# Optimization experiments

Hardware: AMD Instinct MI355X
Metric: run time of the kernel (lower is better)

The kernel has to match this reference:

```python
import jax, jax.numpy as jnp
import numpy as np

H = 32   # rnn_hidden_dim * num_directions
L = 2    # num_layers
F = 1    # num_features
B, T = 2048, 1024


def _xavier(key, shape):
    lim = np.sqrt(6.0 / (shape[0] + shape[1])).astype(np.float32)
    return jax.random.uniform(key, shape, jnp.float32, -lim, lim)


def _lstm_uniform(key, shape):
    lim = np.float32(1.0 / np.sqrt(H))
    return jax.random.uniform(key, shape, jnp.float32, -lim, lim)


def setup_inputs() -> dict:
    key = jax.random.key(0)
    ks = jax.random.split(key, 12)
    return {
        "padded_sequence": jax.random.normal(ks[0], (B, T, F), jnp.float32),
        "z": jax.random.normal(ks[1], (B, H), jnp.float32),
        "lengths": jnp.full((B,), T, jnp.int32),
        # LSTM layer 0 (input size F)
        "w_ih0": _lstm_uniform(ks[2], (4 * H, F)),
        "w_hh0": _lstm_uniform(ks[3], (4 * H, H)),
        "b_ih0": _lstm_uniform(ks[4], (4 * H,)).reshape(4 * H),
        "b_hh0": _lstm_uniform(ks[5], (4 * H,)).reshape(4 * H),
        # LSTM layer 1 (input size H)
        "w_ih1": _lstm_uniform(ks[6], (4 * H, H)),
        "w_hh1": _lstm_uniform(ks[7], (4 * H, H)),
        "b_ih1": _lstm_uniform(ks[8], (4 * H,)).reshape(4 * H),
        "b_hh1": _lstm_uniform(ks[9], (4 * H,)).reshape(4 * H),
        # output projection (xavier weight, bias filled 0.01 per _init_weights)
        "w_out": _xavier(ks[10], (F, H)),
        "b_out": jnp.full((F,), 0.01, jnp.float32),
    }


def _cell(x, h, c, w_ih, w_hh, b):
    # PyTorch LSTM gate order: i, f, g, o
    gates = x @ w_ih.T + h @ w_hh.T + b  # (B, 4H)
    i, f, g, o = jnp.split(gates, 4, axis=-1)
    c_new = jax.nn.sigmoid(f) * c + jax.nn.sigmoid(i) * jnp.tanh(g)
    h_new = jax.nn.sigmoid(o) * jnp.tanh(c_new)
    return h_new, c_new


def reference(padded_sequence, z, lengths, w_ih0, w_hh0, b_ih0, b_hh0,
              w_ih1, w_hh1, b_ih1, b_hh1, w_out, b_out):
    b_sz, n_steps, f = padded_sequence.shape
    b0 = b_ih0 + b_hh0
    b1 = b_ih1 + b_hh1
    pred0 = jnp.zeros((b_sz, f), padded_sequence.dtype)
    # hidden = (z.repeat(L,1,1), z.repeat(L,1,1)): both layers' h and c start as z
    init = (pred0, z, z, z, z)

    def step(carry, _):
        pred, h0, c0, h1, c1 = carry
        h0n, c0n = _cell(pred, h0, c0, w_ih0, w_hh0, b0)
        h1n, c1n = _cell(h0n, h1, c1, w_ih1, w_hh1, b1)
        pred_n = h1n @ w_out.T + b_out  # (B, F)
        return (pred_n, h0n, c0n, h1n, c1n), pred_n

    _, preds = jax.lax.scan(step, init, None, length=n_steps)  # (T, B, F)
    recovered = jnp.transpose(preds, (1, 0, 2))  # (B, T, F)
    loss = jnp.mean((padded_sequence - recovered) ** 2)
    return loss, recovered
```

## Files before the change

kernel.cpp:

```cpp
#include <hip/hip_runtime.h>

#define NB 2048
#define NT 1024

typedef _Float16 half2_t __attribute__((ext_vector_type(2)));
union F4H { float4 f; half2_t h[4]; };

__device__ __forceinline__ float sig_fast(float x) {
    return __builtin_amdgcn_rcpf(1.0f + __builtin_amdgcn_exp2f(-1.4426950408889634f * x));
}
__device__ __forceinline__ float tanh_fast(float x) {
    return fmaf(2.0f, __builtin_amdgcn_rcpf(1.0f + __builtin_amdgcn_exp2f(-2.8853900817779268f * x)), -1.0f);
}

__global__ void zero_loss_kernel(float* out) { out[0] = 0.0f; }

#define LD4(P, i) (*(const float4*)&(P)[i])
#define FDOT(acc, w, hh) acc = __builtin_amdgcn_fdot2((w), (hh), (acc), false)
#define PINH(v) asm volatile("" : "+v"(v))

#define CVTQ(n0, n1, p, i) { float4 r_ = LD4(p, i); \
  n0.x=(_Float16)r_.x; n0.y=(_Float16)r_.y; n1.x=(_Float16)r_.z; n1.y=(_Float16)r_.w; }

#define DECL_ROWH(n, src, row) \
  half2_t n##0,n##1,n##2,n##3,n##4,n##5,n##6,n##7,n##8,n##9,n##10,n##11,n##12,n##13,n##14,n##15; \
  CVTQ(n##0, n##1, src,(row)*32+ 0) CVTQ(n##2, n##3, src,(row)*32+ 4) \
  CVTQ(n##4, n##5, src,(row)*32+ 8) CVTQ(n##6, n##7, src,(row)*32+12) \
  CVTQ(n##8, n##9, src,(row)*32+16) CVTQ(n##10,n##11,src,(row)*32+20) \
  CVTQ(n##12,n##13,src,(row)*32+24) CVTQ(n##14,n##15,src,(row)*32+28) \
  PINH(n##0); PINH(n##1); PINH(n##2); PINH(n##3); PINH(n##4); PINH(n##5); PINH(n##6); PINH(n##7); \
  PINH(n##8); PINH(n##9); PINH(n##10); PINH(n##11); PINH(n##12); PINH(n##13); PINH(n##14); PINH(n##15);

#define DOT16(a0, a1, n, U0, U1, U2, U3) \
  FDOT(a0, n##0,  (U0).h[0]); FDOT(a1, n##1,  (U0).h[1]); \
  FDOT(a0, n##2,  (U0).h[2]); FDOT(a1, n##3,  (U0).h[3]); \
  FDOT(a0, n##4,  (U1).h[0]); FDOT(a1, n##5,  (U1).h[1]); \
  FDOT(a0, n##6,  (U1).h[2]); FDOT(a1, n##7,  (U1).h[3]); \
  FDOT(a0, n##8,  (U2).h[0]); FDOT(a1, n##9,  (U2).h[1]); \
  FDOT(a0, n##10, (U2).h[2]); FDOT(a1, n##11, (U2).h[3]); \
  FDOT(a0, n##12, (U3).h[0]); FDOT(a1, n##13, (U3).h[1]); \
  FDOT(a0, n##14, (U3).h[2]); FDOT(a1, n##15, (U3).h[3]);

__global__ __launch_bounds__(128) __attribute__((amdgpu_waves_per_eu(4, 4)))
void decoder_lstm_kernel(const float* __restrict__ seq,
                         const float* __restrict__ z,
                         const float* __restrict__ w_ih0,
                         const float* __restrict__ w_hh0,
                         const float* __restrict__ b_ih0,
                         const float* __restrict__ b_hh0,
                         const float* __restrict__ w_ih1,
                         const float* __restrict__ w_hh1,
                         const float* __restrict__ b_ih1,
                         const float* __restrict__ b_hh1,
                         const float* __restrict__ w_out,
                         const float* __restrict__ b_out,
                         float* __restrict__ out)
{
    const int tid = threadIdx.x;
    const int w   = tid >> 6;
    const int l   = tid & 63;
    const int q   = l >> 4;
    const int u   = 16 * w + (l & 15);
    const int R   = q * 32 + u;
    const int b   = blockIdx.x;

    __shared__ __align__(16) _Float16 h0buf[2][32];
    __shared__ __align__(16) _Float16 h1buf[2][32];
    __shared__ float pb[2];

    DECL_ROWH(w0, w_hh0, R)
    DECL_ROWH(wi, w_ih1, R)
    DECL_ROWH(wh, w_hh1, R)

    const float wih0R = w_ih0[R];
    const float bias0 = b_ih0[R] + b_hh0[R];
    const float bias1 = b_ih1[R] + b_hh1[R];

    const float m2 = (q == 2) ? 1.0f : 0.0f;
    const float eM = (q == 2) ? -2.8853900817779268f : -1.4426950408889634f;

    const float wOutL = (l < 16) ? w_out[u] : 0.0f;
    const float bOut  = b_out[0];

    const float cz = z[(size_t)b * 32 + u];
    float c0 = cz, c1 = cz;
    if (l < 16) { h0buf[0][u] = (_Float16)cz; h1buf[0][u] = (_Float16)cz; }
    float pred = 0.0f, sse = 0.0f, xreg = 0.0f;

    const float* seq_b = seq + (size_t)b * NT;
    float* out_b = out + 1 + (size_t)b * NT;

    __syncthreads();

    for (int t = 0; t < NT; ++t) {
        const int par = t & 1;
        if (w == 0 && (t & 63) == 0) xreg = seq_b[t + l];

        F4H U0, U1, U2, U3;
        {
            const float4* p0 = (const float4*)h0buf[par];
            U0.f = p0[0]; U1.f = p0[1]; U2.f = p0[2]; U3.f = p0[3];
        }

        float a0 = fmaf(pred, wih0R, bias0), a1 = 0.0f;
        DOT16(a0, a1, w0, U0, U1, U2, U3);
        float v  = a0 + a1;
        float s  = __builtin_amdgcn_rcpf(1.0f + __builtin_amdgcn_exp2f(eM * v));
        float av = fmaf(m2, s - 1.0f, s);

        float x16 = __shfl_xor(av, 16);
        float x32 = __shfl_xor(av, 32);
        float x48 = __shfl_xor(av, 48);
        c0 = fmaf(x16, c0, av * x32);
        float h0n = x48 * tanh_fast(c0);
        if (l < 16) h0buf[par ^ 1][u] = (_Float16)h0n;
        __syncthreads();

        F4H V0, V1, V2, V3, X0, X1, X2, X3;
        {
            const float4* p  = (const float4*)h0buf[par ^ 1];
            const float4* p1 = (const float4*)h1buf[par];
            V0.f = p[0];  V1.f = p[1];  V2.f = p[2];  V3.f = p[3];
            X0.f = p1[0]; X1.f = p1[1]; X2.f = p1[2]; X3.f = p1[3];
        }
        float d0 = bias1, d1 = 0.0f, d2 = 0.0f, d3 = 0.0f;
        DOT16(d0, d1, wi, V0, V1, V2, V3);
        DOT16(d2, d3, wh, X0, X1, X2, X3);
        float v1  = (d0 + d1) + (d2 + d3);
        float s1  = __builtin_amdgcn_rcpf(1.0f + __builtin_amdgcn_exp2f(eM * v1));
        float av1 = fmaf(m2, s1 - 1.0f, s1);

        float y16 = __shfl_xor(av1, 16);
        float y32 = __shfl_xor(av1, 32);
        float y48 = __shfl_xor(av1, 48);
        c1 = fmaf(y16, c1, av1 * y32);
        float h1n = y48 * tanh_fast(c1);
        if (l < 16) h1buf[par ^ 1][u] = (_Float16)h1n;

        float term = wOutL * h1n;
        term += __shfl_xor(term, 1);
        term += __shfl_xor(term, 2);
        term += __shfl_xor(term, 4);
        term += __shfl_xor(term, 8);
        if (l == 0) pb[w] = term;
        __syncthreads();

        pred = bOut + pb[0] + pb[1];

        if (w == 0) {
            out_b[t] = pred;
            float d    = xreg - pred;
            float dsel = ((t & 63) == l) ? d : 0.0f;
            sse = fmaf(dsel, d, sse);
        }
    }

    if (w == 0) {
        sse += __shfl_xor(sse, 1);
        sse += __shfl_xor(sse, 2);
        sse += __shfl_xor(sse, 4);
        sse += __shfl_xor(sse, 8);
        sse += __shfl_xor(sse, 16);
        sse += __shfl_xor(sse, 32);
        if (l == 0) atomicAdd(out, sse * (1.0f / ((float)NB * (float)NT)));
    }
}

extern "C" void kernel_launch(void* const* d_in, const int* in_sizes, int n_in,
                              void* d_out, int out_size, void* d_ws, size_t ws_size,
                              hipStream_t stream) {
    const float* seq   = (const float*)d_in[0];
    const float* z     = (const float*)d_in[1];
    const float* w_ih0 = (const float*)d_in[3];
    const float* w_hh0 = (const float*)d_in[4];
    const float* b_ih0 = (const float*)d_in[5];
    const float* b_hh0 = (const float*)d_in[6];
    const float* w_ih1 = (const float*)d_in[7];
    const float* w_hh1 = (const float*)d_in[8];
    const float* b_ih1 = (const float*)d_in[9];
    const float* b_hh1 = (const float*)d_in[10];
    const float* w_out = (const float*)d_in[11];
    const float* b_out = (const float*)d_in[12];
    float* out = (float*)d_out;

    hipLaunchKernelGGL(zero_loss_kernel, dim3(1), dim3(1), 0, stream, out);
    hipLaunchKernelGGL(decoder_lstm_kernel, dim3(NB), dim3(128), 0, stream,
                       seq, z, w_ih0, w_hh0, b_ih0, b_hh0,
                       w_ih1, w_hh1, b_ih1, b_hh1, w_out, b_out, out);
}
```

Measured before the change: 1.140 ms.

## Stream fp16 recurrent weights from global each step instead of pinning in registers

Adds a prep kernel that converts the three recurrent weight matrices to fp16 and packs them per gate row into a workspace blob. The main kernel then reloads each row's 96 halves from global/L1 every timestep instead of holding 48 packed registers for the whole loop. The aim is to cut VGPR pressure, at the price of extra per-step memory loads on the serial critical path. The asm barrier on the pointer keeps the compiler from hoisting the loads out of the loop.

```diff
diff --git a/kernel.cpp b/kernel.cpp
--- a/kernel.cpp
+++ b/kernel.cpp
@@ -6,54 +6,41 @@
 typedef _Float16 half2_t __attribute__((ext_vector_type(2)));
 union F4H { float4 f; half2_t h[4]; };
 
-__device__ __forceinline__ float sig_fast(float x) {
-    return __builtin_amdgcn_rcpf(1.0f + __builtin_amdgcn_exp2f(-1.4426950408889634f * x));
-}
 __device__ __forceinline__ float tanh_fast(float x) {
     return fmaf(2.0f, __builtin_amdgcn_rcpf(1.0f + __builtin_amdgcn_exp2f(-2.8853900817779268f * x)), -1.0f);
 }
 
 __global__ void zero_loss_kernel(float* out) { out[0] = 0.0f; }
 
-#define LD4(P, i) (*(const float4*)&(P)[i])
+__global__ void prep_weights(const float* __restrict__ w_hh0,
+                             const float* __restrict__ w_ih1,
+                             const float* __restrict__ w_hh1,
+                             _Float16* __restrict__ blob) {
+    int i = blockIdx.x * blockDim.x + threadIdx.x;
+    if (i < 128 * 32) {
+        int R = i >> 5, k = i & 31;
+        blob[R * 96 +      k] = (_Float16)w_hh0[i];
+        blob[R * 96 + 32 + k] = (_Float16)w_ih1[i];
+        blob[R * 96 + 64 + k] = (_Float16)w_hh1[i];
+    }
+}
+
 #define FDOT(acc, w, hh) acc = __builtin_amdgcn_fdot2((w), (hh), (acc), false)
-#define PINH(v) asm volatile("" : "+v"(v))
-
-#define CVTQ(n0, n1, p, i) { float4 r_ = LD4(p, i); \
-  n0.x=(_Float16)r_.x; n0.y=(_Float16)r_.y; n1.x=(_Float16)r_.z; n1.y=(_Float16)r_.w; }
-
-#define DECL_ROWH(n, src, row) \
-  half2_t n##0,n##1,n##2,n##3,n##4,n##5,n##6,n##7,n##8,n##9,n##10,n##11,n##12,n##13,n##14,n##15; \
-  CVTQ(n##0, n##1, src,(row)*32+ 0) CVTQ(n##2, n##3, src,(row)*32+ 4) \
-  CVTQ(n##4, n##5, src,(row)*32+ 8) CVTQ(n##6, n##7, src,(row)*32+12) \
-  CVTQ(n##8, n##9, src,(row)*32+16) CVTQ(n##10,n##11,src,(row)*32+20) \
-  CVTQ(n##12,n##13,src,(row)*32+24) CVTQ(n##14,n##15,src,(row)*32+28) \
-  PINH(n##0); PINH(n##1); PINH(n##2); PINH(n##3); PINH(n##4); PINH(n##5); PINH(n##6); PINH(n##7); \
-  PINH(n##8); PINH(n##9); PINH(n##10); PINH(n##11); PINH(n##12); PINH(n##13); PINH(n##14); PINH(n##15);
-
-#define DOT16(a0, a1, n, U0, U1, U2, U3) \
-  FDOT(a0, n##0,  (U0).h[0]); FDOT(a1, n##1,  (U0).h[1]); \
-  FDOT(a0, n##2,  (U0).h[2]); FDOT(a1, n##3,  (U0).h[3]); \
-  FDOT(a0, n##4,  (U1).h[0]); FDOT(a1, n##5,  (U1).h[1]); \
-  FDOT(a0, n##6,  (U1).h[2]); FDOT(a1, n##7,  (U1).h[3]); \
-  FDOT(a0, n##8,  (U2).h[0]); FDOT(a1, n##9,  (U2).h[1]); \
-  FDOT(a0, n##10, (U2).h[2]); FDOT(a1, n##11, (U2).h[3]); \
-  FDOT(a0, n##12, (U3).h[0]); FDOT(a1, n##13, (U3).h[1]); \
-  FDOT(a0, n##14, (U3).h[2]); FDOT(a1, n##15, (U3).h[3]);
+#define DOT4W(a0, a1, W, U) \
+  FDOT(a0, (W).h[0], (U).h[0]); FDOT(a1, (W).h[1], (U).h[1]); \
+  FDOT(a0, (W).h[2], (U).h[2]); FDOT(a1, (W).h[3], (U).h[3]);
 
 __global__ __launch_bounds__(128) __attribute__((amdgpu_waves_per_eu(4, 4)))
 void decoder_lstm_kernel(const float* __restrict__ seq,
                          const float* __restrict__ z,
                          const float* __restrict__ w_ih0,
-                         const float* __restrict__ w_hh0,
                          const float* __restrict__ b_ih0,
                          const float* __restrict__ b_hh0,
-                         const float* __restrict__ w_ih1,
-                         const float* __restrict__ w_hh1,
                          const float* __restrict__ b_ih1,
                          const float* __restrict__ b_hh1,
                          const float* __restrict__ w_out,
                          const float* __restrict__ b_out,
+                         const _Float16* __restrict__ blob,
                          float* __restrict__ out)
 {
     const int tid = threadIdx.x;
@@ -68,9 +55,7 @@
     __shared__ __align__(16) _Float16 h1buf[2][32];
     __shared__ float pb[2];
 
-    DECL_ROWH(w0, w_hh0, R)
-    DECL_ROWH(wi, w_ih1, R)
-    DECL_ROWH(wh, w_hh1, R)
+    const _Float16* wp = blob + R * 96;
 
     const float wih0R = w_ih0[R];
     const float bias0 = b_ih0[R] + b_hh0[R];
@@ -94,19 +79,34 @@
 
     for (int t = 0; t < NT; ++t) {
         const int par = t & 1;
+
+        const _Float16* wq = wp;
+        asm("" : "+v"(wq));
+
         if (w == 0 && (t & 63) == 0) xreg = seq_b[t + l];
 
+        F4H Wa, Wb, Wc, Wd;
+        Wa.f = *(const float4*)(wq +  0);
+        Wb.f = *(const float4*)(wq +  8);
+        Wc.f = *(const float4*)(wq + 16);
+        Wd.f = *(const float4*)(wq + 24);
+
         F4H U0, U1, U2, U3;
-        {
-            const float4* p0 = (const float4*)h0buf[par];
-            U0.f = p0[0]; U1.f = p0[1]; U2.f = p0[2]; U3.f = p0[3];
-        }
+        { const float4* p0 = (const float4*)h0buf[par];
+          U0.f = p0[0]; U1.f = p0[1]; U2.f = p0[2]; U3.f = p0[3]; }
 
         float a0 = fmaf(pred, wih0R, bias0), a1 = 0.0f;
-        DOT16(a0, a1, w0, U0, U1, U2, U3);
+        DOT4W(a0, a1, Wa, U0); DOT4W(a0, a1, Wb, U1);
+        DOT4W(a0, a1, Wc, U2); DOT4W(a0, a1, Wd, U3);
         float v  = a0 + a1;
         float s  = __builtin_amdgcn_rcpf(1.0f + __builtin_amdgcn_exp2f(eM * v));
         float av = fmaf(m2, s - 1.0f, s);
+
+        F4H Ia, Ib, Ic, Id;
+        Ia.f = *(const float4*)(wq + 32);
+        Ib.f = *(const float4*)(wq + 40);
+        Ic.f = *(const float4*)(wq + 48);
+        Id.f = *(const float4*)(wq + 56);
 
         float x16 = __shfl_xor(av, 16);
         float x32 = __shfl_xor(av, 32);
@@ -116,16 +116,24 @@
         if (l < 16) h0buf[par ^ 1][u] = (_Float16)h0n;
         __syncthreads();
 
+        F4H Ha, Hb, Hc, Hd;
+        Ha.f = *(const float4*)(wq + 64);
+        Hb.f = *(const float4*)(wq + 72);
+        Hc.f = *(const float4*)(wq + 80);
+        Hd.f = *(const float4*)(wq + 88);
+
         F4H V0, V1, V2, V3, X0, X1, X2, X3;
-        {
-            const float4* p  = (const float4*)h0buf[par ^ 1];
-            const float4* p1 = (const float4*)h1buf[par];
-            V0.f = p[0];  V1.f = p[1];  V2.f = p[2];  V3.f = p[3];
-            X0.f = p1[0]; X1.f = p1[1]; X2.f = p1[2]; X3.f = p1[3];
-        }
-        float d0 = bias1, d1 = 0.0f, d2 = 0.0f, d3 = 0.0f;
-        DOT16(d0, d1, wi, V0, V1, V2, V3);
-        DOT16(d2, d3, wh, X0, X1, X2, X3);
+        { const float4* p  = (const float4*)h0buf[par ^ 1];
+          const float4* p1 = (const float4*)h1buf[par];
+          V0.f = p[0];  V1.f = p[1];  V2.f = p[2];  V3.f = p[3];
+          X0.f = p1[0]; X1.f = p1[1]; X2.f = p1[2]; X3.f = p1[3]; }
+
+        float d0 = bias1, d1 = 0.0f;
+        DOT4W(d0, d1, Ia, V0); DOT4W(d0, d1, Ib, V1);
+        DOT4W(d0, d1, Ic, V2); DOT4W(d0, d1, Id, V3);
+        float d2 = 0.0f, d3 = 0.0f;
+        DOT4W(d2, d3, Ha, X0); DOT4W(d2, d3, Hb, X1);
+        DOT4W(d2, d3, Hc, X2); DOT4W(d2, d3, Hd, X3);
         float v1  = (d0 + d1) + (d2 + d3);
         float s1  = __builtin_amdgcn_rcpf(1.0f + __builtin_amdgcn_exp2f(eM * v1));
         float av1 = fmaf(m2, s1 - 1.0f, s1);
@@ -182,9 +190,12 @@
     const float* w_out = (const float*)d_in[11];
     const float* b_out = (const float*)d_in[12];
     float* out = (float*)d_out;
+    _Float16* blob = (_Float16*)d_ws;
 
     hipLaunchKernelGGL(zero_loss_kernel, dim3(1), dim3(1), 0, stream, out);
+    hipLaunchKernelGGL(prep_weights, dim3(16), dim3(256), 0, stream,
+                       w_hh0, w_ih1, w_hh1, blob);
     hipLaunchKernelGGL(decoder_lstm_kernel, dim3(NB), dim3(128), 0, stream,
-                       seq, z, w_ih0, w_hh0, b_ih0, b_hh0,
-                       w_ih1, w_hh1, b_ih1, b_hh1, w_out, b_out, out);
-}
+                       seq, z, w_ih0, b_ih0, b_hh0, b_ih1, b_hh1,
+                       w_out, b_out, blob, out);
+}
```

Result: slower. 2.733 ms (+139.7%).

## Split each gate row's K dimension across two lanes with 256-thread blocks

Applied to the files above, without the earlier changes.

Each block now uses four waves instead of two. Each gate row's 32-element dot product is split into two 16-element halves held by paired lanes, and the halves are combined with an extra cross-lane shuffle before the activations. This halves the per-thread weight registers and dot-product chain length, shortening the serial per-timestep latency. The cost is twice the threads per batch element, an extra shuffle per layer, and more waves taking part in each block barrier.

```diff
diff --git a/kernel.cpp b/kernel.cpp
--- a/kernel.cpp
+++ b/kernel.cpp
@@ -6,9 +6,6 @@
 typedef _Float16 half2_t __attribute__((ext_vector_type(2)));
 union F4H { float4 f; half2_t h[4]; };
 
-__device__ __forceinline__ float sig_fast(float x) {
-    return __builtin_amdgcn_rcpf(1.0f + __builtin_amdgcn_exp2f(-1.4426950408889634f * x));
-}
 __device__ __forceinline__ float tanh_fast(float x) {
     return fmaf(2.0f, __builtin_amdgcn_rcpf(1.0f + __builtin_amdgcn_exp2f(-2.8853900817779268f * x)), -1.0f);
 }
@@ -17,31 +14,22 @@
 
 #define LD4(P, i) (*(const float4*)&(P)[i])
 #define FDOT(acc, w, hh) acc = __builtin_amdgcn_fdot2((w), (hh), (acc), false)
-#define PINH(v) asm volatile("" : "+v"(v))
 
 #define CVTQ(n0, n1, p, i) { float4 r_ = LD4(p, i); \
   n0.x=(_Float16)r_.x; n0.y=(_Float16)r_.y; n1.x=(_Float16)r_.z; n1.y=(_Float16)r_.w; }
 
-#define DECL_ROWH(n, src, row) \
-  half2_t n##0,n##1,n##2,n##3,n##4,n##5,n##6,n##7,n##8,n##9,n##10,n##11,n##12,n##13,n##14,n##15; \
-  CVTQ(n##0, n##1, src,(row)*32+ 0) CVTQ(n##2, n##3, src,(row)*32+ 4) \
-  CVTQ(n##4, n##5, src,(row)*32+ 8) CVTQ(n##6, n##7, src,(row)*32+12) \
-  CVTQ(n##8, n##9, src,(row)*32+16) CVTQ(n##10,n##11,src,(row)*32+20) \
-  CVTQ(n##12,n##13,src,(row)*32+24) CVTQ(n##14,n##15,src,(row)*32+28) \
-  PINH(n##0); PINH(n##1); PINH(n##2); PINH(n##3); PINH(n##4); PINH(n##5); PINH(n##6); PINH(n##7); \
-  PINH(n##8); PINH(n##9); PINH(n##10); PINH(n##11); PINH(n##12); PINH(n##13); PINH(n##14); PINH(n##15);
+#define DECL_HALFROW(n, src, row, kb) \
+  half2_t n##0,n##1,n##2,n##3,n##4,n##5,n##6,n##7; \
+  CVTQ(n##0, n##1, src, (row)*32 + (kb) + 0)  CVTQ(n##2, n##3, src, (row)*32 + (kb) + 4) \
+  CVTQ(n##4, n##5, src, (row)*32 + (kb) + 8)  CVTQ(n##6, n##7, src, (row)*32 + (kb) + 12)
 
-#define DOT16(a0, a1, n, U0, U1, U2, U3) \
-  FDOT(a0, n##0,  (U0).h[0]); FDOT(a1, n##1,  (U0).h[1]); \
-  FDOT(a0, n##2,  (U0).h[2]); FDOT(a1, n##3,  (U0).h[3]); \
-  FDOT(a0, n##4,  (U1).h[0]); FDOT(a1, n##5,  (U1).h[1]); \
-  FDOT(a0, n##6,  (U1).h[2]); FDOT(a1, n##7,  (U1).h[3]); \
-  FDOT(a0, n##8,  (U2).h[0]); FDOT(a1, n##9,  (U2).h[1]); \
-  FDOT(a0, n##10, (U2).h[2]); FDOT(a1, n##11, (U2).h[3]); \
-  FDOT(a0, n##12, (U3).h[0]); FDOT(a1, n##13, (U3).h[1]); \
-  FDOT(a0, n##14, (U3).h[2]); FDOT(a1, n##15, (U3).h[3]);
+#define DOT8(a0, a1, n, U0, U1) \
+  FDOT(a0, n##0, (U0).h[0]); FDOT(a1, n##1, (U0).h[1]); \
+  FDOT(a0, n##2, (U0).h[2]); FDOT(a1, n##3, (U0).h[3]); \
+  FDOT(a0, n##4, (U1).h[0]); FDOT(a1, n##5, (U1).h[1]); \
+  FDOT(a0, n##6, (U1).h[2]); FDOT(a1, n##7, (U1).h[3]);
 
-__global__ __launch_bounds__(128) __attribute__((amdgpu_waves_per_eu(4, 4)))
+__global__ __launch_bounds__(256)
 void decoder_lstm_kernel(const float* __restrict__ seq,
                          const float* __restrict__ z,
                          const float* __restrict__ w_ih0,
@@ -60,31 +48,34 @@
     const int w   = tid >> 6;
     const int l   = tid & 63;
     const int q   = l >> 4;
-    const int u   = 16 * w + (l & 15);
+    const int h   = (l >> 3) & 1;
+    const int e   = l & 7;
+    const int u   = 8 * w + e;
     const int R   = q * 32 + u;
+    const int kb  = 16 * h;
     const int b   = blockIdx.x;
 
     __shared__ __align__(16) _Float16 h0buf[2][32];
     __shared__ __align__(16) _Float16 h1buf[2][32];
-    __shared__ float pb[2];
+    __shared__ float pb[4];
 
-    DECL_ROWH(w0, w_hh0, R)
-    DECL_ROWH(wi, w_ih1, R)
-    DECL_ROWH(wh, w_hh1, R)
+    DECL_HALFROW(w0, w_hh0, R, kb)
+    DECL_HALFROW(wi, w_ih1, R, kb)
+    DECL_HALFROW(wh, w_hh1, R, kb)
 
-    const float wih0R = w_ih0[R];
-    const float bias0 = b_ih0[R] + b_hh0[R];
-    const float bias1 = b_ih1[R] + b_hh1[R];
+    const float bias0L = h ? 0.0f : (b_ih0[R] + b_hh0[R]);
+    const float bias1L = h ? 0.0f : (b_ih1[R] + b_hh1[R]);
+    const float wih0L  = h ? 0.0f : w_ih0[R];
 
     const float m2 = (q == 2) ? 1.0f : 0.0f;
     const float eM = (q == 2) ? -2.8853900817779268f : -1.4426950408889634f;
 
-    const float wOutL = (l < 16) ? w_out[u] : 0.0f;
+    const float wOutL = (l < 8) ? w_out[u] : 0.0f;
     const float bOut  = b_out[0];
 
     const float cz = z[(size_t)b * 32 + u];
     float c0 = cz, c1 = cz;
-    if (l < 16) { h0buf[0][u] = (_Float16)cz; h1buf[0][u] = (_Float16)cz; }
+    if (l < 8) { h0buf[0][u] = (_Float16)cz; h1buf[0][u] = (_Float16)cz; }
     float pred = 0.0f, sse = 0.0f, xreg = 0.0f;
 
     const float* seq_b = seq + (size_t)b * NT;
@@ -96,15 +87,14 @@
         const int par = t & 1;
         if (w == 0 && (t & 63) == 0) xreg = seq_b[t + l];
 
-        F4H U0, U1, U2, U3;
-        {
-            const float4* p0 = (const float4*)h0buf[par];
-            U0.f = p0[0]; U1.f = p0[1]; U2.f = p0[2]; U3.f = p0[3];
-        }
+        F4H U0, U1;
+        U0.f = *(const float4*)&h0buf[par][kb];
+        U1.f = *(const float4*)&h0buf[par][kb + 8];
 
-        float a0 = fmaf(pred, wih0R, bias0), a1 = 0.0f;
-        DOT16(a0, a1, w0, U0, U1, U2, U3);
-        float v  = a0 + a1;
+        float a0 = fmaf(pred, wih0L, bias0L), a1 = 0.0f;
+        DOT8(a0, a1, w0, U0, U1);
+        float v = a0 + a1;
+        v += __shfl_xor(v, 8);
         float s  = __builtin_amdgcn_rcpf(1.0f + __builtin_amdgcn_exp2f(eM * v));
         float av = fmaf(m2, s - 1.0f, s);
 
@@ -113,20 +103,20 @@
         float x48 = __shfl_xor(av, 48);
         c0 = fmaf(x16, c0, av * x32);
         float h0n = x48 * tanh_fast(c0);
-        if (l < 16) h0buf[par ^ 1][u] = (_Float16)h0n;
+        if (l < 8) h0buf[par ^ 1][u] = (_Float16)h0n;
         __syncthreads();
 
-        F4H V0, V1, V2, V3, X0, X1, X2, X3;
-        {
-            const float4* p  = (const float4*)h0buf[par ^ 1];
-            const float4* p1 = (const float4*)h1buf[par];
-            V0.f = p[0];  V1.f = p[1];  V2.f = p[2];  V3.f = p[3];
-            X0.f = p1[0]; X1.f = p1[1]; X2.f = p1[2]; X3.f = p1[3];
-        }
-        float d0 = bias1, d1 = 0.0f, d2 = 0.0f, d3 = 0.0f;
-        DOT16(d0, d1, wi, V0, V1, V2, V3);
-        DOT16(d2, d3, wh, X0, X1, X2, X3);
-        float v1  = (d0 + d1) + (d2 + d3);
+        F4H V0, V1, X0, X1;
+        V0.f = *(const float4*)&h0buf[par ^ 1][kb];
+        V1.f = *(const float4*)&h0buf[par ^ 1][kb + 8];
+        X0.f = *(const float4*)&h1buf[par][kb];
+        X1.f = *(const float4*)&h1buf[par][kb + 8];
+
+        float d0 = bias1L, d1 = 0.0f;
+        DOT8(d0, d1, wi, V0, V1);
+        DOT8(d0, d1, wh, X0, X1);
+        float v1 = d0 + d1;
+        v1 += __shfl_xor(v1, 8);
         float s1  = __builtin_amdgcn_rcpf(1.0f + __builtin_amdgcn_exp2f(eM * v1));
         float av1 = fmaf(m2, s1 - 1.0f, s1);
 
@@ -135,17 +125,16 @@
         float y48 = __shfl_xor(av1, 48);
         c1 = fmaf(y16, c1, av1 * y32);
         float h1n = y48 * tanh_fast(c1);
-        if (l < 16) h1buf[par ^ 1][u] = (_Float16)h1n;
+        if (l < 8) h1buf[par ^ 1][u] = (_Float16)h1n;
 
         float term = wOutL * h1n;
         term += __shfl_xor(term, 1);
         term += __shfl_xor(term, 2);
         term += __shfl_xor(term, 4);
-        term += __shfl_xor(term, 8);
         if (l == 0) pb[w] = term;
         __syncthreads();
 
-        pred = bOut + pb[0] + pb[1];
+        pred = bOut + ((pb[0] + pb[1]) + (pb[2] + pb[3]));
 
         if (w == 0) {
             out_b[t] = pred;
@@ -184,7 +173,7 @@
     float* out = (float*)d_out;
 
     hipLaunchKernelGGL(zero_loss_kernel, dim3(1), dim3(1), 0, stream, out);
-    hipLaunchKernelGGL(decoder_lstm_kernel, dim3(NB), dim3(128), 0, stream,
+    hipLaunchKernelGGL(decoder_lstm_kernel, dim3(NB), dim3(256), 0, stream,
                        seq, z, w_ih0, w_hh0, b_ih0, b_hh0,
                        w_ih1, w_hh1, b_ih1, b_hh1, w_out, b_out, out);
 }
```

Measured after the change: 1.874 ms. 64.4% more time.

## Recompute output projection redundantly per thread from shared h1, use fp32 weights

Applied to the files above, without the earlier changes.

Drops the per-step cross-wave shuffle reduction of the output projection and its extra shared slot. Instead, every thread recomputes pred from the shared h1 vector at the start of the next step, using w_out held in scalar registers, and folds b_out into the layer-0 bias. It also switches the recurrent state and weights from fp16 fdot2 to fp32 FMAs, which doubles the multiply work and register use but removes conversion and precision loss. The last prediction is computed after the loop.

```diff
diff --git a/kernel.cpp b/kernel.cpp
--- a/kernel.cpp
+++ b/kernel.cpp
@@ -3,43 +3,21 @@
 #define NB 2048
 #define NT 1024
 
-typedef _Float16 half2_t __attribute__((ext_vector_type(2)));
-union F4H { float4 f; half2_t h[4]; };
-
-__device__ __forceinline__ float sig_fast(float x) {
-    return __builtin_amdgcn_rcpf(1.0f + __builtin_amdgcn_exp2f(-1.4426950408889634f * x));
-}
+typedef float vf4 __attribute__((ext_vector_type(4)));
+
 __device__ __forceinline__ float tanh_fast(float x) {
     return fmaf(2.0f, __builtin_amdgcn_rcpf(1.0f + __builtin_amdgcn_exp2f(-2.8853900817779268f * x)), -1.0f);
 }
 
+__device__ __forceinline__ float sgpr_f(float v) {
+    return __int_as_float(__builtin_amdgcn_readfirstlane(__float_as_int(v)));
+}
+
 __global__ void zero_loss_kernel(float* out) { out[0] = 0.0f; }
 
-#define LD4(P, i) (*(const float4*)&(P)[i])
-#define FDOT(acc, w, hh) acc = __builtin_amdgcn_fdot2((w), (hh), (acc), false)
-#define PINH(v) asm volatile("" : "+v"(v))
-
-#define CVTQ(n0, n1, p, i) { float4 r_ = LD4(p, i); \
-  n0.x=(_Float16)r_.x; n0.y=(_Float16)r_.y; n1.x=(_Float16)r_.z; n1.y=(_Float16)r_.w; }
-
-#define DECL_ROWH(n, src, row) \
-  half2_t n##0,n##1,n##2,n##3,n##4,n##5,n##6,n##7,n##8,n##9,n##10,n##11,n##12,n##13,n##14,n##15; \
-  CVTQ(n##0, n##1, src,(row)*32+ 0) CVTQ(n##2, n##3, src,(row)*32+ 4) \
-  CVTQ(n##4, n##5, src,(row)*32+ 8) CVTQ(n##6, n##7, src,(row)*32+12) \
-  CVTQ(n##8, n##9, src,(row)*32+16) CVTQ(n##10,n##11,src,(row)*32+20) \
-  CVTQ(n##12,n##13,src,(row)*32+24) CVTQ(n##14,n##15,src,(row)*32+28) \
-  PINH(n##0); PINH(n##1); PINH(n##2); PINH(n##3); PINH(n##4); PINH(n##5); PINH(n##6); PINH(n##7); \
-  PINH(n##8); PINH(n##9); PINH(n##10); PINH(n##11); PINH(n##12); PINH(n##13); PINH(n##14); PINH(n##15);
-
-#define DOT16(a0, a1, n, U0, U1, U2, U3) \
-  FDOT(a0, n##0,  (U0).h[0]); FDOT(a1, n##1,  (U0).h[1]); \
-  FDOT(a0, n##2,  (U0).h[2]); FDOT(a1, n##3,  (U0).h[3]); \
-  FDOT(a0, n##4,  (U1).h[0]); FDOT(a1, n##5,  (U1).h[1]); \
-  FDOT(a0, n##6,  (U1).h[2]); FDOT(a1, n##7,  (U1).h[3]); \
-  FDOT(a0, n##8,  (U2).h[0]); FDOT(a1, n##9,  (U2).h[1]); \
-  FDOT(a0, n##10, (U2).h[2]); FDOT(a1, n##11, (U2).h[3]); \
-  FDOT(a0, n##12, (U3).h[0]); FDOT(a1, n##13, (U3).h[1]); \
-  FDOT(a0, n##14, (U3).h[2]); FDOT(a1, n##15, (U3).h[3]);
+#define MAC4(a0, a1, W, H) \
+  a0 = fmaf((W).x, (H).x, a0); a1 = fmaf((W).y, (H).y, a1); \
+  a0 = fmaf((W).z, (H).z, a0); a1 = fmaf((W).w, (H).w, a1);
 
 __global__ __launch_bounds__(128) __attribute__((amdgpu_waves_per_eu(4, 4)))
 void decoder_lstm_kernel(const float* __restrict__ seq,
@@ -64,28 +42,32 @@
     const int R   = q * 32 + u;
     const int b   = blockIdx.x;
 
-    __shared__ __align__(16) _Float16 h0buf[2][32];
-    __shared__ __align__(16) _Float16 h1buf[2][32];
-    __shared__ float pb[2];
-
-    DECL_ROWH(w0, w_hh0, R)
-    DECL_ROWH(wi, w_ih1, R)
-    DECL_ROWH(wh, w_hh1, R)
-
-    const float wih0R = w_ih0[R];
-    const float bias0 = b_ih0[R] + b_hh0[R];
-    const float bias1 = b_ih1[R] + b_hh1[R];
+    __shared__ __align__(16) float h0buf[2][32];
+    __shared__ __align__(16) float h1buf[2][32];
+
+    const volatile vf4* W0 = (const volatile vf4*)&w_hh0[R * 32];
+    const volatile vf4* WI = (const volatile vf4*)&w_ih1[R * 32];
+    const volatile vf4* WH = (const volatile vf4*)&w_hh1[R * 32];
+    vf4 w00=W0[0], w01=W0[1], w02=W0[2], w03=W0[3], w04=W0[4], w05=W0[5], w06=W0[6], w07=W0[7];
+    vf4 wi0=WI[0], wi1=WI[1], wi2=WI[2], wi3=WI[3], wi4=WI[4], wi5=WI[5], wi6=WI[6], wi7=WI[7];
+    vf4 wh0=WH[0], wh1=WH[1], wh2=WH[2], wh3=WH[3], wh4=WH[4], wh5=WH[5], wh6=WH[6], wh7=WH[7];
+
+    float so[32];
+#pragma unroll
+    for (int k = 0; k < 32; ++k) so[k] = sgpr_f(w_out[k]);
+
+    const float wih0R  = w_ih0[R];
+    const float bOut   = b_out[0];
+    const float bias0f = fmaf(wih0R, bOut, b_ih0[R] + b_hh0[R]);
+    const float bias1  = b_ih1[R] + b_hh1[R];
 
     const float m2 = (q == 2) ? 1.0f : 0.0f;
     const float eM = (q == 2) ? -2.8853900817779268f : -1.4426950408889634f;
 
-    const float wOutL = (l < 16) ? w_out[u] : 0.0f;
-    const float bOut  = b_out[0];
-
     const float cz = z[(size_t)b * 32 + u];
     float c0 = cz, c1 = cz;
-    if (l < 16) { h0buf[0][u] = (_Float16)cz; h1buf[0][u] = (_Float16)cz; }
-    float pred = 0.0f, sse = 0.0f, xreg = 0.0f;
+    if (l < 16) { h0buf[0][u] = cz; h1buf[0][u] = cz; }
+    float sse = 0.0f, xreg = 0.0f;
 
     const float* seq_b = seq + (size_t)b * NT;
     float* out_b = out + 1 + (size_t)b * NT;
@@ -94,17 +76,45 @@
 
     for (int t = 0; t < NT; ++t) {
         const int par = t & 1;
-        if (w == 0 && (t & 63) == 0) xreg = seq_b[t + l];
-
-        F4H U0, U1, U2, U3;
+        const float* h1p = h1buf[par];
+        const float* h0p = h0buf[par];
+
+        float a0 = 0.0f, a1 = 0.0f;
+#pragma unroll
+        for (int kk = 0; kk < 32; kk += 4) {
+            vf4 F = *(const vf4*)&h1p[kk];
+            a0 = fmaf(so[kk + 0], F.x, a0);
+            a1 = fmaf(so[kk + 1], F.y, a1);
+            a0 = fmaf(so[kk + 2], F.z, a0);
+            a1 = fmaf(so[kk + 3], F.w, a1);
+        }
+        const float a  = a0 + a1;
+        const float af = t ? a : -bOut;
+
+        if (w == 0) {
+            if ((t & 63) == 1) xreg = seq_b[(t - 1) + l];
+            if (t) {
+                float predv = a + bOut;
+                out_b[t - 1] = predv;
+                float d  = xreg - predv;
+                float ds = (((t - 1) & 63) == l) ? d : 0.0f;
+                sse = fmaf(ds, d, sse);
+            }
+        }
+
+        float g0 = 0.f, g1 = 0.f, g2 = 0.f, g3 = 0.f;
         {
-            const float4* p0 = (const float4*)h0buf[par];
-            U0.f = p0[0]; U1.f = p0[1]; U2.f = p0[2]; U3.f = p0[3];
-        }
-
-        float a0 = fmaf(pred, wih0R, bias0), a1 = 0.0f;
-        DOT16(a0, a1, w0, U0, U1, U2, U3);
-        float v  = a0 + a1;
+            vf4 F;
+            F = *(const vf4*)&h0p[0];  MAC4(g0, g1, w00, F);
+            F = *(const vf4*)&h0p[4];  MAC4(g2, g3, w01, F);
+            F = *(const vf4*)&h0p[8];  MAC4(g0, g1, w02, F);
+            F = *(const vf4*)&h0p[12]; MAC4(g2, g3, w03, F);
+            F = *(const vf4*)&h0p[16]; MAC4(g0, g1, w04, F);
+            F = *(const vf4*)&h0p[20]; MAC4(g2, g3, w05, F);
+            F = *(const vf4*)&h0p[24]; MAC4(g0, g1, w06, F);
+            F = *(const vf4*)&h0p[28]; MAC4(g2, g3, w07, F);
+        }
+        float v  = ((g0 + g1) + (g2 + g3)) + fmaf(wih0R, af, bias0f);
         float s  = __builtin_amdgcn_rcpf(1.0f + __builtin_amdgcn_exp2f(eM * v));
         float av = fmaf(m2, s - 1.0f, s);
 
@@ -113,20 +123,31 @@
         float x48 = __shfl_xor(av, 48);
         c0 = fmaf(x16, c0, av * x32);
         float h0n = x48 * tanh_fast(c0);
-        if (l < 16) h0buf[par ^ 1][u] = (_Float16)h0n;
+        if (l < 16) h0buf[par ^ 1][u] = h0n;
         __syncthreads();
 
-        F4H V0, V1, V2, V3, X0, X1, X2, X3;
+        const float* n0p = h0buf[par ^ 1];
+        float d0 = 0.f, d1 = 0.f, d2 = 0.f, d3 = 0.f;
         {
-            const float4* p  = (const float4*)h0buf[par ^ 1];
-            const float4* p1 = (const float4*)h1buf[par];
-            V0.f = p[0];  V1.f = p[1];  V2.f = p[2];  V3.f = p[3];
-            X0.f = p1[0]; X1.f = p1[1]; X2.f = p1[2]; X3.f = p1[3];
-        }
-        float d0 = bias1, d1 = 0.0f, d2 = 0.0f, d3 = 0.0f;
-        DOT16(d0, d1, wi, V0, V1, V2, V3);
-        DOT16(d2, d3, wh, X0, X1, X2, X3);
-        float v1  = (d0 + d1) + (d2 + d3);
+            vf4 F;
+            F = *(const vf4*)&n0p[0];  MAC4(d0, d1, wi0, F);
+            F = *(const vf4*)&h1p[0];  MAC4(d2, d3, wh0, F);
+            F = *(const vf4*)&n0p[4];  MAC4(d0, d1, wi1, F);
+            F = *(const vf4*)&h1p[4];  MAC4(d2, d3, wh1, F);
+            F = *(const vf4*)&n0p[8];  MAC4(d0, d1, wi2, F);
+            F = *(const vf4*)&h1p[8];  MAC4(d2, d3, wh2, F);
+            F = *(const vf4*)&n0p[12]; MAC4(d0, d1, wi3, F);
+            F = *(const vf4*)&h1p[12]; MAC4(d2, d3, wh3, F);
+            F = *(const vf4*)&n0p[16]; MAC4(d0, d1, wi4, F);
+            F = *(const vf4*)&h1p[16]; MAC4(d2, d3, wh4, F);
+            F = *(const vf4*)&n0p[20]; MAC4(d0, d1, wi5, F);
+            F = *(const vf4*)&h1p[20]; MAC4(d2, d3, wh5, F);
+            F = *(const vf4*)&n0p[24]; MAC4(d0, d1, wi6, F);
+            F = *(const vf4*)&h1p[24]; MAC4(d2, d3, wh6, F);
+            F = *(const vf4*)&n0p[28]; MAC4(d0, d1, wi7, F);
+            F = *(const vf4*)&h1p[28]; MAC4(d2, d3, wh7, F);
+        }
+        float v1  = ((d0 + d1) + (d2 + d3)) + bias1;
         float s1  = __builtin_amdgcn_rcpf(1.0f + __builtin_amdgcn_exp2f(eM * v1));
         float av1 = fmaf(m2, s1 - 1.0f, s1);
 
@@ -135,34 +156,36 @@
         float y48 = __shfl_xor(av1, 48);
         c1 = fmaf(y16, c1, av1 * y32);
         float h1n = y48 * tanh_fast(c1);
-        if (l < 16) h1buf[par ^ 1][u] = (_Float16)h1n;
-
-        float term = wOutL * h1n;
-        term += __shfl_xor(term, 1);
-        term += __shfl_xor(term, 2);
-        term += __shfl_xor(term, 4);
-        term += __shfl_xor(term, 8);
-        if (l == 0) pb[w] = term;
+        if (l < 16) h1buf[par ^ 1][u] = h1n;
         __syncthreads();
-
-        pred = bOut + pb[0] + pb[1];
-
+    }
+
+    {
+        const float* h1f = h1buf[0];
+        float a0 = 0.0f, a1 = 0.0f;
+#pragma unroll
+        for (int kk = 0; kk < 32; kk += 4) {
+            vf4 F = *(const vf4*)&h1f[kk];
+            a0 = fmaf(so[kk + 0], F.x, a0);
+            a1 = fmaf(so[kk + 1], F.y, a1);
+            a0 = fmaf(so[kk + 2], F.z, a0);
+            a1 = fmaf(so[kk + 3], F.w, a1);
+        }
         if (w == 0) {
-            out_b[t] = pred;
-            float d    = xreg - pred;
-            float dsel = ((t & 63) == l) ? d : 0.0f;
-            sse = fmaf(dsel, d, sse);
-        }
-    }
-
-    if (w == 0) {
-        sse += __shfl_xor(sse, 1);
-        sse += __shfl_xor(sse, 2);
-        sse += __shfl_xor(sse, 4);
-        sse += __shfl_xor(sse, 8);
-        sse += __shfl_xor(sse, 16);
-        sse += __shfl_xor(sse, 32);
-        if (l == 0) atomicAdd(out, sse * (1.0f / ((float)NB * (float)NT)));
+            float predv = (a0 + a1) + bOut;
+            out_b[NT - 1] = predv;
+            float d  = xreg - predv;
+            float ds = (l == 63) ? d : 0.0f;
+            sse = fmaf(ds, d, sse);
+
+            sse += __shfl_xor(sse, 1);
+            sse += __shfl_xor(sse, 2);
+            sse += __shfl_xor(sse, 4);
+            sse += __shfl_xor(sse, 8);
+            sse += __shfl_xor(sse, 16);
+            sse += __shfl_xor(sse, 32);
+            if (l == 0) atomicAdd(out, sse * (1.0f / ((float)NB * (float)NT)));
+        }
     }
 }
 
```

After: 2.067 ms. +81.3%, slower.
